# Performance work log

Hardware: AMD Instinct MI355X
Metric: run time of the kernel (lower is better)

Reference implementation:

```python
import jax, jax.numpy as jnp
import numpy as np

OUT_H = OUT_W = 7
SCALE = 0.25
SR = 2  # sampling_ratio


def setup_inputs() -> dict:
    key = jax.random.key(0)
    k1, k2, k3, k4, k5, k6 = jax.random.split(key, 6)
    B, C, H, W = 2, 256, 200, 304
    N = 1000
    inputs = jax.random.normal(k1, (B, C, H, W), dtype=jnp.float32)
    # rois: (batch_idx, cx, cy, w, h, angle_deg) in IMAGE coords (scale back by 1/SCALE)
    bidx = jax.random.randint(k2, (N,), 0, B).astype(jnp.float32)
    cx = jax.random.uniform(k3, (N,), minval=0.0, maxval=W / SCALE)
    cy = jax.random.uniform(k4, (N,), minval=0.0, maxval=H / SCALE)
    wh = jax.random.uniform(k5, (N, 2), minval=16.0, maxval=256.0)
    ang = jax.random.uniform(k6, (N,), minval=-90.0, maxval=90.0)
    rois = jnp.concatenate([bidx[:, None], cx[:, None], cy[:, None], wh, ang[:, None]], axis=1)
    return {"inputs": inputs, "rois": rois}


def _roi_align_rotated(feats, rois):
    B, C, H, W = feats.shape
    N = rois.shape[0]
    offset = 0.5  # aligned=True continuous-coordinate convention
    bidx = rois[:, 0].astype(jnp.int32)
    cw = rois[:, 1] * SCALE - offset
    ch = rois[:, 2] * SCALE - offset
    rw = rois[:, 3] * SCALE
    rh = rois[:, 4] * SCALE
    theta = rois[:, 5] * (jnp.pi / 180.0)
    cos_t, sin_t = jnp.cos(theta), jnp.sin(theta)

    bin_h = rh / OUT_H
    bin_w = rw / OUT_W
    # fused (bin, subsample) coordinate: t[j] = ph + (iy+0.5)/SR for j = ph*SR+iy
    t_y = (jnp.arange(OUT_H * SR, dtype=feats.dtype) + 0.5) / SR  # [GH]
    t_x = (jnp.arange(OUT_W * SR, dtype=feats.dtype) + 0.5) / SR  # [GW]
    yy = -rh[:, None] / 2.0 + t_y[None, :] * bin_h[:, None]  # [N,GH] roi-local
    xx = -rw[:, None] / 2.0 + t_x[None, :] * bin_w[:, None]  # [N,GW]

    # rotate into feature-map coords
    y = yy[:, :, None] * cos_t[:, None, None] - xx[:, None, :] * sin_t[:, None, None] + ch[:, None, None]
    x = yy[:, :, None] * sin_t[:, None, None] + xx[:, None, :] * cos_t[:, None, None] + cw[:, None, None]

    empty = (y < -1.0) | (y > H) | (x < -1.0) | (x > W)
    y = jnp.clip(y, 0.0, None)
    x = jnp.clip(x, 0.0, None)
    y_low = jnp.clip(jnp.floor(y).astype(jnp.int32), 0, H - 1)
    x_low = jnp.clip(jnp.floor(x).astype(jnp.int32), 0, W - 1)
    y_high = jnp.minimum(y_low + 1, H - 1)
    x_high = jnp.minimum(x_low + 1, W - 1)
    ly = jnp.clip(y - y_low.astype(y.dtype), 0.0, 1.0)
    lx = jnp.clip(x - x_low.astype(x.dtype), 0.0, 1.0)
    hy, hx = 1.0 - ly, 1.0 - lx

    b = bidx[:, None, None]  # [N,1,1] broadcasts with [N,GH,GW] index arrays
    v1 = feats[b, :, y_low, x_low]    # [N,GH,GW,C]
    v2 = feats[b, :, y_low, x_high]
    v3 = feats[b, :, y_high, x_low]
    v4 = feats[b, :, y_high, x_high]

    w1 = (hy * hx)[..., None]
    w2 = (hy * lx)[..., None]
    w3 = (ly * hx)[..., None]
    w4 = (ly * lx)[..., None]
    val = w1 * v1 + w2 * v2 + w3 * v3 + w4 * v4  # [N,GH,GW,C]
    val = jnp.where(empty[..., None], 0.0, val)

    # average the SRxSR samples within each output bin
    val = val.reshape(rois.shape[0], OUT_H, SR, OUT_W, SR, C).mean(axis=(2, 4))
    return jnp.transpose(val, (0, 3, 1, 2))  # [N,C,OUT_H,OUT_W]


def reference(inputs, rois):
    return _roi_align_rotated(inputs, rois)
```

## Files before the change

kernel.cpp:

```cpp
#include <hip/hip_runtime.h>
#include <math.h>

constexpr int Bn = 2, Cn = 256, Hn = 200, Wn = 304, Nroi = 1000;
constexpr int OH = 7, OW = 7, SRn = 2;
constexpr int NS = OH * SRn;
constexpr int NP = NS * NS;
constexpr int NBIN = OH * OW;
constexpr int HWn = Hn * Wn;
constexpr float SCALE = 0.25f;

__device__ __forceinline__ void compute_desc(const float* __restrict__ r, int p,
                                             int& idx, int& dx, int& dyW,
                                             float4& w) {
  float cw = r[1] * SCALE - 0.5f;
  float ch = r[2] * SCALE - 0.5f;
  float rw = r[3] * SCALE;
  float rh = r[4] * SCALE;
  float theta = r[5] * 0.017453292519943295f;
  float cs = cosf(theta), sn = sinf(theta);
  float bin_h = rh * (1.0f / OH);
  float bin_w = rw * (1.0f / OW);
  int ki = p / NS;
  int kj = p - ki * NS;
  float ty = ((float)ki + 0.5f) * (1.0f / SRn);
  float tx = ((float)kj + 0.5f) * (1.0f / SRn);
  float yy = -0.5f * rh + ty * bin_h;
  float xx = -0.5f * rw + tx * bin_w;
  float y = yy * cs - xx * sn + ch;
  float x = yy * sn + xx * cs + cw;
  bool empty = (y < -1.0f) || (y > (float)Hn) || (x < -1.0f) || (x > (float)Wn);
  y = fmaxf(y, 0.0f);
  x = fmaxf(x, 0.0f);
  int yl = min(max((int)floorf(y), 0), Hn - 1);
  int xl = min(max((int)floorf(x), 0), Wn - 1);
  int yh = min(yl + 1, Hn - 1);
  int xh = min(xl + 1, Wn - 1);
  float ly = fminf(fmaxf(y - (float)yl, 0.0f), 1.0f);
  float lx = fminf(fmaxf(x - (float)xl, 0.0f), 1.0f);
  float hy = 1.0f - ly, hx = 1.0f - lx;
  if (empty) {
    w.x = w.y = w.z = w.w = 0.0f;
  } else {
    w.x = hy * hx;
    w.y = hy * lx;
    w.z = ly * hx;
    w.w = ly * lx;
  }
  idx = yl * Wn + xl;
  dx = xh - xl;
  dyW = (yh - yl) * Wn;
}

__device__ __forceinline__ unsigned bf16rne(float f) {
  unsigned u = __float_as_uint(f);
  return (u + 0x7fffu + ((u >> 16) & 1u)) >> 16;
}
__device__ __forceinline__ unsigned bf16pack(float lo, float hi) {
  return bf16rne(lo) | (bf16rne(hi) << 16);
}

constexpr int TPX = 64, TCH = 64, LP = TPX + 1;
__global__ __launch_bounds__(256) void transpose_bf16(const float* __restrict__ feats,
                                                      unsigned short* __restrict__ ft) {
  __shared__ float tile[TCH * LP];
  int p0 = blockIdx.x * TPX;
  int c0 = blockIdx.y * TCH;
  int b = blockIdx.z;
  int t = threadIdx.x;
  int px4 = t & 15, ch = t >> 4;
#pragma unroll
  for (int i = 0; i < 4; ++i) {
    int c = ch + 16 * i;
    const float4 v = *(const float4*)(feats + ((size_t)b * Cn + c0 + c) * HWn + p0 + px4 * 4);
    tile[c * LP + px4 * 4 + 0] = v.x;
    tile[c * LP + px4 * 4 + 1] = v.y;
    tile[c * LP + px4 * 4 + 2] = v.z;
    tile[c * LP + px4 * 4 + 3] = v.w;
  }
  __syncthreads();
  int o = t & 7;
  int px8 = t >> 3;
#pragma unroll
  for (int pass = 0; pass < 2; ++pass) {
    int p = px8 + 32 * pass;
    uint4 w4;
    w4.x = bf16pack(tile[(o * 8 + 0) * LP + p], tile[(o * 8 + 1) * LP + p]);
    w4.y = bf16pack(tile[(o * 8 + 2) * LP + p], tile[(o * 8 + 3) * LP + p]);
    w4.z = bf16pack(tile[(o * 8 + 4) * LP + p], tile[(o * 8 + 5) * LP + p]);
    w4.w = bf16pack(tile[(o * 8 + 6) * LP + p], tile[(o * 8 + 7) * LP + p]);
    *(uint4*)((char*)ft + (((size_t)b * HWn + p0 + p) * Cn + c0 + o * 8) * 2) = w4;
  }
}

constexpr int HB1 = 25;
__global__ __launch_bounds__(256, 4) void roi_gather7(const unsigned short* __restrict__ ft,
                                                      const float* __restrict__ rois,
                                                      float* __restrict__ out) {
  __shared__ int4 s_m[NP];
  __shared__ float4 s_w[NP];
  __shared__ __align__(16) float s_out[Cn * HB1];
  int n = blockIdx.x;
  const float* r = rois + (size_t)n * 6;
  int t = threadIdx.x;
  if (t < NP) {
    int idx, dx, dy;
    float4 w;
    compute_desc(r, t, idx, dx, dy, w);
    s_m[t] = make_int4(idx * (Cn * 2), dx * (Cn * 2), dy * (Cn * 2), 0);
    s_w[t] = w;
  }
  __syncthreads();
  int b = (int)r[0];
  int lane = t & 63;
  int wv = t >> 6;
  int k = lane & 31;
  int q = lane >> 5;
  const char* fb = (const char*)ft + (size_t)b * HWn * Cn * 2 + (size_t)k * 16;
  float* ob = out + (size_t)n * Cn * NBIN;

#pragma unroll 1
  for (int ph = 0; ph < 2; ++ph) {
    int b0 = ph ? HB1 : 0;
    int b1 = ph ? NBIN : HB1;
    for (int bin = b0 + wv; bin < b1; bin += 4) {
      int bi = bin / OW;
      int bj = bin - bi * OW;
      int p00 = (bi * 2) * NS + bj * 2;
      float acc0 = 0.f, acc1 = 0.f, acc2 = 0.f, acc3 = 0.f;
      float acc4 = 0.f, acc5 = 0.f, acc6 = 0.f, acc7 = 0.f;
#pragma unroll
      for (int s = 0; s < 4; ++s) {
        int p = p00 + (s >> 1) * NS + (s & 1);
        int4 m = s_m[p];
        float4 w = s_w[p];
        const char* A = fb + m.x + q * m.y;
        uint4 vlo = *(const uint4*)(A);
        uint4 vhi = *(const uint4*)(A + m.z);
        float wlo = q ? w.y : w.x;
        float whi = q ? w.w : w.z;
#define ACC(vv, ww)                                                        \
        acc0 += (ww) * __uint_as_float((vv).x << 16);                      \
        acc1 += (ww) * __uint_as_float((vv).x & 0xffff0000u);              \
        acc2 += (ww) * __uint_as_float((vv).y << 16);                      \
        acc3 += (ww) * __uint_as_float((vv).y & 0xffff0000u);              \
        acc4 += (ww) * __uint_as_float((vv).z << 16);                      \
        acc5 += (ww) * __uint_as_float((vv).z & 0xffff0000u);              \
        acc6 += (ww) * __uint_as_float((vv).w << 16);                      \
        acc7 += (ww) * __uint_as_float((vv).w & 0xffff0000u);
        ACC(vlo, wlo)
        ACC(vhi, whi)
#undef ACC
      }
      acc0 += __shfl_xor(acc0, 32);
      acc1 += __shfl_xor(acc1, 32);
      acc2 += __shfl_xor(acc2, 32);
      acc3 += __shfl_xor(acc3, 32);
      acc4 += __shfl_xor(acc4, 32);
      acc5 += __shfl_xor(acc5, 32);
      acc6 += __shfl_xor(acc6, 32);
      acc7 += __shfl_xor(acc7, 32);
      if (q == 0) {
        int col = bin - b0;
        s_out[(k * 8 + 0) * HB1 + col] = acc0 * 0.25f;
        s_out[(k * 8 + 1) * HB1 + col] = acc1 * 0.25f;
        s_out[(k * 8 + 2) * HB1 + col] = acc2 * 0.25f;
        s_out[(k * 8 + 3) * HB1 + col] = acc3 * 0.25f;
        s_out[(k * 8 + 4) * HB1 + col] = acc4 * 0.25f;
        s_out[(k * 8 + 5) * HB1 + col] = acc5 * 0.25f;
        s_out[(k * 8 + 6) * HB1 + col] = acc6 * 0.25f;
        s_out[(k * 8 + 7) * HB1 + col] = acc7 * 0.25f;
      }
    }
    __syncthreads();
    if (ph == 0) {
#pragma unroll
      for (int i2 = 0; i2 < 25; ++i2) {
        int idx = t + 256 * i2;
        int c = idx / 25;
        int bn = idx - c * 25;
        ob[c * NBIN + bn] = s_out[idx];
      }
    } else {
#pragma unroll
      for (int i2 = 0; i2 < 24; ++i2) {
        int idx = t + 256 * i2;
        int c = idx / 24;
        int bn = idx - c * 24;
        ob[c * NBIN + HB1 + bn] = s_out[c * HB1 + bn];
      }
    }
    __syncthreads();
  }
}

__global__ __launch_bounds__(256) void roi_direct(const float* __restrict__ feats,
                                                  const float* __restrict__ rois,
                                                  float* __restrict__ out) {
  __shared__ int s_idx[NP];
  __shared__ int s_dx[NP];
  __shared__ int s_dy[NP];
  __shared__ float4 s_w[NP];
  int n = blockIdx.x;
  const float* r = rois + (size_t)n * 6;
  int t = threadIdx.x;
  if (t < NP) {
    int idx, dx, dy;
    float4 w;
    compute_desc(r, t, idx, dx, dy, w);
    s_idx[t] = idx;
    s_dx[t] = dx;
    s_dy[t] = dy;
    s_w[t] = w;
  }
  __syncthreads();
  int b = (int)r[0];
  const float* f = feats + ((size_t)b * Cn + t) * HWn;
  float* o = out + ((size_t)n * Cn + t) * NBIN;
  for (int bi = 0; bi < OH; ++bi) {
    for (int bj = 0; bj < OW; ++bj) {
      float acc = 0.0f;
#pragma unroll
      for (int s = 0; s < 4; ++s) {
        int p = (bi * 2 + (s >> 1)) * NS + bj * 2 + (s & 1);
        int idx = s_idx[p];
        int dx = s_dx[p];
        int dy = s_dy[p];
        float4 w = s_w[p];
        acc += w.x * f[idx] + w.y * f[idx + dx] + w.z * f[idx + dy] + w.w * f[idx + dy + dx];
      }
      o[bi * OW + bj] = acc * 0.25f;
    }
  }
}

extern "C" void kernel_launch(void* const* d_in, const int* in_sizes, int n_in,
                              void* d_out, int out_size, void* d_ws, size_t ws_size,
                              hipStream_t stream) {
  const float* feats = (const float*)d_in[0];
  const float* rois = (const float*)d_in[1];
  float* out = (float*)d_out;

  size_t need = (size_t)Bn * HWn * Cn * sizeof(unsigned short);
  if (ws_size >= need) {
    unsigned short* ft = (unsigned short*)d_ws;
    transpose_bf16<<<dim3(HWn / TPX, Cn / TCH, Bn), 256, 0, stream>>>(feats, ft);
    roi_gather7<<<dim3(Nroi), 256, 0, stream>>>(ft, rois, out);
  } else {
    roi_direct<<<Nroi, 256, 0, stream>>>(feats, rois, out);
  }
}
```

Baseline: 278.2 us.

## Sort ROIs by Morton-ordered spatial key and remap blocks per XCD for locality

Adds a single-block bitonic sort that orders ROIs by batch index and a Morton code of their center tile, producing a permutation. The gather kernel reads its ROI through this permutation, and the block-to-ROI mapping is strided by 8 so that the blocks on each XCD get a contiguous run of spatially nearby ROIs. The aim is more L2 reuse of the bf16 feature map between neighbouring ROIs. In exchange it adds an extra small kernel launch on the stream and slightly more workspace.

```diff
diff --git a/kernel.cpp b/kernel.cpp
--- a/kernel.cpp
+++ b/kernel.cpp
@@ -59,6 +59,45 @@
   return bf16rne(lo) | (bf16rne(hi) << 16);
 }
 
+__global__ __launch_bounds__(512) void sort_rois(const float* __restrict__ rois,
+                                                 int* __restrict__ perm) {
+  __shared__ unsigned a[1024];
+  int t = threadIdx.x;
+  for (int i = t; i < 1024; i += 512) {
+    unsigned packed;
+    if (i < Nroi) {
+      const float* r = rois + (size_t)i * 6;
+      int b = (int)r[0];
+      int tx = min(max((int)(r[1] * SCALE * (1.0f / 16.0f)), 0), 31);
+      int ty = min(max((int)(r[2] * SCALE * (1.0f / 16.0f)), 0), 31);
+      unsigned m = 0;
+#pragma unroll
+      for (int bit = 0; bit < 5; ++bit) {
+        m |= (((tx >> bit) & 1u) << (2 * bit)) | (((ty >> bit) & 1u) << (2 * bit + 1));
+      }
+      unsigned key = ((unsigned)b << 10) | m;
+      packed = (key << 10) | (unsigned)i;
+    } else {
+      packed = 0xFFFFFC00u | (unsigned)i;
+    }
+    a[i] = packed;
+  }
+  for (int k = 2; k <= 1024; k <<= 1) {
+    for (int j = k >> 1; j > 0; j >>= 1) {
+      __syncthreads();
+      int i = ((t & ~(j - 1)) << 1) | (t & (j - 1));
+      bool up = ((i & k) == 0);
+      unsigned x = a[i], y = a[i + j];
+      if ((x > y) == up) {
+        a[i] = y;
+        a[i + j] = x;
+      }
+    }
+  }
+  __syncthreads();
+  for (int i = t; i < Nroi; i += 512) perm[i] = (int)(a[i] & 1023u);
+}
+
 constexpr int TPX = 64, TCH = 64, LP = TPX + 1;
 __global__ __launch_bounds__(256) void transpose_bf16(const float* __restrict__ feats,
                                                       unsigned short* __restrict__ ft) {
@@ -93,13 +132,15 @@
 }
 
 constexpr int HB1 = 25;
-__global__ __launch_bounds__(256, 4) void roi_gather7(const unsigned short* __restrict__ ft,
+__global__ __launch_bounds__(256, 4) void roi_gather8(const unsigned short* __restrict__ ft,
                                                       const float* __restrict__ rois,
+                                                      const int* __restrict__ perm,
                                                       float* __restrict__ out) {
   __shared__ int4 s_m[NP];
   __shared__ float4 s_w[NP];
   __shared__ __align__(16) float s_out[Cn * HB1];
-  int n = blockIdx.x;
+  int bid = blockIdx.x;
+  int n = perm[((bid & 7) * (Nroi / 8)) + (bid >> 3)];
   const float* r = rois + (size_t)n * 6;
   int t = threadIdx.x;
   if (t < NP) {
@@ -240,11 +281,14 @@
   const float* rois = (const float*)d_in[1];
   float* out = (float*)d_out;
 
-  size_t need = (size_t)Bn * HWn * Cn * sizeof(unsigned short);
+  size_t ftBytes = (size_t)Bn * HWn * Cn * sizeof(unsigned short);
+  size_t need = ftBytes + 4096;
   if (ws_size >= need) {
     unsigned short* ft = (unsigned short*)d_ws;
+    int* perm = (int*)((char*)d_ws + ftBytes);
+    sort_rois<<<1, 512, 0, stream>>>(rois, perm);
     transpose_bf16<<<dim3(HWn / TPX, Cn / TCH, Bn), 256, 0, stream>>>(feats, ft);
-    roi_gather7<<<dim3(Nroi), 256, 0, stream>>>(ft, rois, out);
+    roi_gather8<<<dim3(Nroi), 256, 0, stream>>>(ft, rois, perm, out);
   } else {
     roi_direct<<<Nroi, 256, 0, stream>>>(feats, rois, out);
   }
```

After: 281.4 us. Within noise of the previous version (+1.2%).
